# Performance work log

Hardware: AMD Instinct MI355X
Metric: run time of the kernel (lower is better)

Reference implementation:

```python
import jax, jax.numpy as jnp
import numpy as np

EMB = 768
HEADS = 3
HD = EMB // HEADS  # 256
B, S = 4, 2048


def setup_inputs() -> dict:
    key = jax.random.key(0)
    ks = jax.random.split(key, 8)
    inputs_for_keys = jax.random.normal(ks[0], (B, S, EMB), dtype=jnp.float32)
    inputs_for_values = jax.random.normal(ks[1], (B, S, EMB), dtype=jnp.float32)
    inputs_for_queries = jax.random.normal(ks[2], (B, S, EMB), dtype=jnp.float32)
    # stacked per-head projection weights: [heads, emb, head_dim]
    # original uses 'random_uniform' init (small uniform); scale ~0.05
    Wk = jax.random.uniform(ks[3], (HEADS, EMB, HD), jnp.float32, -0.05, 0.05)
    Wv = jax.random.uniform(ks[4], (HEADS, EMB, HD), jnp.float32, -0.05, 0.05)
    Wq = jax.random.uniform(ks[5], (HEADS, EMB, HD), jnp.float32, -0.05, 0.05)
    Wo = jax.random.normal(ks[6], (EMB, EMB), dtype=jnp.float32) * (1.0 / np.sqrt(EMB))
    bo = jnp.zeros((EMB,), dtype=jnp.float32)
    return {
        "inputs_for_keys": inputs_for_keys,
        "inputs_for_values": inputs_for_values,
        "inputs_for_queries": inputs_for_queries,
        "Wk": Wk, "Wv": Wv, "Wq": Wq, "Wo": Wo, "bo": bo,
    }


def reference(inputs_for_keys, inputs_for_values, inputs_for_queries, Wk, Wv, Wq, Wo, bo):
    # per-head projections, batched over heads: [b, h, s, f]
    K = jnp.einsum('bse,hef->bhsf', inputs_for_keys, Wk)
    V = jnp.einsum('bse,hef->bhsf', inputs_for_values, Wv)
    Q = jnp.einsum('bse,hef->bhsf', inputs_for_queries, Wq)

    seq_k = inputs_for_keys.shape[1]
    seq_q = inputs_for_queries.shape[1]
    # NOTE: original scales by sqrt(window_size_keys) (seq len), not sqrt(d_k)
    scale = jnp.sqrt(jnp.float32(seq_k))

    scores = jnp.einsum('bhqf,bhkf->bhqk', Q, K) / scale
    # causal mask: -inf strictly above the diagonal (j > i)
    mask = jnp.triu(jnp.full((seq_q, seq_k), -jnp.inf, dtype=scores.dtype), k=1)
    scores = scores + mask

    attn = jax.nn.softmax(scores, axis=-1)  # [b,h,q,k]
    heads = jnp.einsum('bhqk,bhkf->bhqf', attn, V)

    # concat heads along feature dim: [b, q, heads*hd]
    b, h, q, f = heads.shape
    concat = heads.transpose(0, 2, 1, 3).reshape(b, q, h * f)
    return concat @ Wo + bo
```

## Files before the change

### kernel.cpp

```cpp
#include <hip/hip_runtime.h>

#define BATCH 4
#define NHEADS 3
#define SEQ 2048
#define HDIM 256
#define EMBD 768
#define MTOT (BATCH*SEQ)
#define WSZ (NHEADS*EMBD*HDIM)

typedef unsigned short u16x8 __attribute__((ext_vector_type(8)));
typedef unsigned short u16x4 __attribute__((ext_vector_type(4)));
typedef __bf16 bf16x8 __attribute__((ext_vector_type(8)));
typedef float fx4 __attribute__((ext_vector_type(4)));

__device__ __forceinline__ unsigned short f2bf(float x) {
    union { float f; unsigned int u; } v; v.f = x;
    unsigned int r = v.u + 0x7fffu + ((v.u >> 16) & 1u);
    return (unsigned short)(r >> 16);
}

__device__ __forceinline__ fx4 mfma16(u16x8 a, u16x8 b, fx4 c) {
    return __builtin_amdgcn_mfma_f32_16x16x32_bf16(
        __builtin_bit_cast(bf16x8, a), __builtin_bit_cast(bf16x8, b), c, 0, 0, 0);
}

__device__ __forceinline__ void gl_lds16(const unsigned short* g, unsigned short* l) {
    __builtin_amdgcn_global_load_lds(
        (const __attribute__((address_space(1))) unsigned int*)g,
        (__attribute__((address_space(3))) unsigned int*)l, 16, 0, 0);
}

__device__ const unsigned char attn_sched[48] = {
    124,125, 63, 120,121, 116,117, 59, 112,113, 108,109, 55, 104,105,
    100,101, 51,  96, 97,  92, 93, 47,  88, 89,  84, 85, 43,  80, 81,
     76, 77, 39,  72, 73,  68, 69, 35,  64, 65,  31, 27, 23, 19, 15,
     11,  7,  3
};

__global__ __launch_bounds__(256) void castAw_kernel(
    const float* __restrict__ Ak, const float* __restrict__ Av,
    const float* __restrict__ Aq,
    const float* __restrict__ Wk, const float* __restrict__ Wv,
    const float* __restrict__ Wq, const float* __restrict__ Wo,
    unsigned short* __restrict__ Abf, unsigned short* __restrict__ Wt,
    unsigned short* __restrict__ Wot)
{
    __shared__ float tile[64][65];
    int bx = blockIdx.x;
    if (bx < 9216) {
        int e = (bx * 256 + threadIdx.x) * 8;
        int t = e / (MTOT * EMBD);
        int r = e - t * (MTOT * EMBD);
        const float* A = (t == 0) ? Ak : (t == 1) ? Av : Aq;
        const fx4* s = (const fx4*)(A + r);
        fx4 v0 = s[0], v1 = s[1];
        u16x8 o;
        o[0]=f2bf(v0[0]); o[1]=f2bf(v0[1]); o[2]=f2bf(v0[2]); o[3]=f2bf(v0[3]);
        o[4]=f2bf(v1[0]); o[5]=f2bf(v1[1]); o[6]=f2bf(v1[2]); o[7]=f2bf(v1[3]);
        *(u16x8*)(Abf + e) = o;
        return;
    }
    int z = bx - 9216;
    const float* src; unsigned short* dst;
    int src_ld, dst_ld, e0, f0;
    if (z < 432) {
        int t = z / 144, rem = z - t * 144;
        int h = rem / 48, tl = rem - h * 48;
        e0 = (tl % 12) * 64; f0 = (tl / 12) * 64;
        const float* W = (t == 0) ? Wk : (t == 1) ? Wv : Wq;
        src = W + h * 768 * 256; src_ld = 256;
        dst = Wt + t * WSZ + h * 256 * 768; dst_ld = 768;
    } else {
        int zz = z - 432;
        e0 = (zz % 12) * 64; f0 = (zz / 12) * 64;
        src = Wo; src_ld = 768;
        dst = Wot; dst_ld = 768;
    }
    int tx = threadIdx.x & 63, ty4 = threadIdx.x >> 6;
    #pragma unroll
    for (int i = 0; i < 16; ++i) {
        int r = ty4 + i * 4;
        tile[r][tx] = src[(e0 + r) * src_ld + f0 + tx];
    }
    __syncthreads();
    #pragma unroll
    for (int i = 0; i < 16; ++i) {
        int r = ty4 + i * 4;
        dst[(f0 + r) * dst_ld + e0 + tx] = f2bf(tile[tx][r]);
    }
}

__global__ __launch_bounds__(256) void proj_kernel(
    const unsigned short* __restrict__ Abf, const unsigned short* __restrict__ Wt,
    unsigned short* __restrict__ Kg, unsigned short* __restrict__ Vg,
    unsigned short* __restrict__ Qg)
{
    __shared__ alignas(16) unsigned short S[17408];
    unsigned short* As = S;
    unsigned short* Bs = S + 8192;

    int z = blockIdx.z;
    const unsigned short* A = Abf + z * (MTOT * EMBD);
    int m0 = blockIdx.x * 128;
    int h = blockIdx.y >> 1, fbase = (blockIdx.y & 1) * 128;
    const unsigned short* W = Wt + z * WSZ + (h * 256 + fbase) * EMBD;

    int tid = threadIdx.x;
    int w = tid >> 6, ln = tid & 63;
    int lane16 = ln & 15, quad = ln >> 4;
    int mw = (w & 1) * 64, nw = (w >> 1) * 64;

    fx4 acc[4][4];
    #pragma unroll
    for (int i = 0; i < 4; ++i)
        #pragma unroll
        for (int j = 0; j < 4; ++j) acc[i][j] = (fx4){0.f, 0.f, 0.f, 0.f};

    const unsigned short *Ag[4], *Wg[4];
    #pragma unroll
    for (int i = 0; i < 4; ++i) {
        int c = tid + 256 * i;
        int R = c >> 3;
        int So = (((c & 7) ^ (R & 7)) * 8);
        Ag[i] = A + (m0 + R) * EMBD + So;
        Wg[i] = W + R * EMBD + So;
    }

    int ca0 = ((quad + 0) ^ (lane16 & 7)) * 8;
    int ca1 = ((quad + 4) ^ (lane16 & 7)) * 8;

    for (int kb = 0; kb < EMBD; kb += 64) {
        __syncthreads();
        #pragma unroll
        for (int i = 0; i < 4; ++i) {
            gl_lds16(Ag[i] + kb, &As[(tid + 256 * i) * 8]);
            gl_lds16(Wg[i] + kb, &Bs[(tid + 256 * i) * 8]);
        }
        __syncthreads();

        #pragma unroll
        for (int kh = 0; kh < 2; ++kh) {
            int co = kh ? ca1 : ca0;
            u16x8 af[4], bf[4];
            #pragma unroll
            for (int i = 0; i < 4; ++i) {
                af[i] = *(const u16x8*)&As[(mw + i * 16 + lane16) * 64 + co];
                bf[i] = *(const u16x8*)&Bs[(nw + i * 16 + lane16) * 64 + co];
            }
            #pragma unroll
            for (int i = 0; i < 4; ++i)
                #pragma unroll
                for (int j = 0; j < 4; ++j)
                    acc[i][j] = mfma16(af[i], bf[j], acc[i][j]);
        }
    }

    __syncthreads();
    int b = m0 >> 11, sq0 = m0 & 2047;

    if (z == 1) {
        #pragma unroll
        for (int i = 0; i < 4; ++i)
            #pragma unroll
            for (int j = 0; j < 4; ++j) {
                int fl = nw + j * 16 + lane16;
                int ml = mw + i * 16 + quad * 4;
                u16x4 pk;
                pk[0] = f2bf(acc[i][j][0]); pk[1] = f2bf(acc[i][j][1]);
                pk[2] = f2bf(acc[i][j][2]); pk[3] = f2bf(acc[i][j][3]);
                *(u16x4*)&S[fl * 136 + ml] = pk;
            }
        __syncthreads();
        int fl = tid >> 1, mseg = (tid & 1) * 64;
        const unsigned short* srcp = &S[fl * 136 + mseg];
        unsigned short* dstp = Vg + ((b * NHEADS + h) * HDIM + fbase + fl) * SEQ + sq0 + mseg;
        #pragma unroll
        for (int c = 0; c < 8; ++c)
            *(u16x8*)(dstp + c * 8) = *(const u16x8*)(srcp + c * 8);
    } else {
        #pragma unroll
        for (int i = 0; i < 4; ++i)
            #pragma unroll
            for (int j = 0; j < 4; ++j) {
                int fl = nw + j * 16 + lane16;
                int ml = mw + i * 16 + quad * 4;
                #pragma unroll
                for (int r = 0; r < 4; ++r)
                    S[(ml + r) * 136 + fl] = f2bf(acc[i][j][r]);
            }
        __syncthreads();
        unsigned short* dst0 = (z == 0) ? Kg : Qg;
        int ml = tid >> 1, fseg = (tid & 1) * 64;
        const unsigned short* srcp = &S[ml * 136 + fseg];
        unsigned short* dstp = dst0 + ((b * NHEADS + h) * SEQ + sq0 + ml) * HDIM + fbase + fseg;
        #pragma unroll
        for (int c = 0; c < 8; ++c)
            *(u16x8*)(dstp + c * 8) = *(const u16x8*)(srcp + c * 8);
    }
}

__global__ __launch_bounds__(256) void attn_kernel(
    const unsigned short* __restrict__ Kg, const unsigned short* __restrict__ Vg,
    const unsigned short* __restrict__ Qg, unsigned short* __restrict__ heads,
    float* __restrict__ Opart, float* __restrict__ Lpart)
{
    __shared__ alignas(16) unsigned short Ks[32 * 264];
    __shared__ alignas(16) unsigned short Vs[256 * 40];

    int bx = blockIdx.x;
    int bh = bx % 12;
    int ent = attn_sched[bx / 12];
    int qt = ent >> 2, kc = ent & 3;
    int tid = threadIdx.x;
    int w = tid >> 6, ln = tid & 63;
    int lane16 = ln & 15, quad = ln >> 4;
    int q0w = qt * 64 + w * 16;

    const unsigned short* Kbase = Kg + bh * (SEQ * HDIM);
    const unsigned short* Vbase = Vg + bh * (SEQ * HDIM);
    const unsigned short* Qbase = Qg + bh * (SEQ * HDIM);

    u16x8 qf[8];
    {
        const unsigned short* qrow = Qbase + (q0w + lane16) * HDIM + quad * 8;
        #pragma unroll
        for (int c = 0; c < 8; ++c) qf[c] = *(const u16x8*)(qrow + c * 32);
    }

    fx4 o[16];
    #pragma unroll
    for (int i = 0; i < 16; ++i) o[i] = (fx4){0.f, 0.f, 0.f, 0.f};
    float lsum = 0.f;

    const float Cs2 = 0.03188010519640429f;

    int t0, t1;
    if (kc == 3) { t0 = 0; t1 = 2 * qt + 2; }
    else         { t0 = kc * (qt + 1); t1 = t0 + qt + 1; }

    int ksrow = tid >> 3, kseg = tid & 7;
    const unsigned short* kstage = Kbase + ksrow * HDIM + kseg * 32;
    const unsigned short* vstage = Vbase + tid * SEQ;

    u16x8 kreg[4], vreg[4];
    {
        int k0 = t0 * 32;
        #pragma unroll
        for (int j = 0; j < 4; ++j) {
            kreg[j] = *(const u16x8*)(kstage + k0 * HDIM + j * 8);
            vreg[j] = *(const u16x8*)(vstage + k0 + j * 8);
        }
    }

    for (int kt = t0; kt < t1; ++kt) {
        __syncthreads();
        {
            u16x8* kd = (u16x8*)&Ks[ksrow * 264 + kseg * 32];
            kd[0] = kreg[0]; kd[1] = kreg[1]; kd[2] = kreg[2]; kd[3] = kreg[3];
            u16x8* vd = (u16x8*)&Vs[tid * 40];
            vd[0] = vreg[0]; vd[1] = vreg[1]; vd[2] = vreg[2]; vd[3] = vreg[3];
        }
        if (kt + 1 < t1) {
            int k0n = (kt + 1) * 32;
            #pragma unroll
            for (int j = 0; j < 4; ++j) {
                kreg[j] = *(const u16x8*)(kstage + k0n * HDIM + j * 8);
                vreg[j] = *(const u16x8*)(vstage + k0n + j * 8);
            }
        }
        __syncthreads();

        int k0 = kt * 32;
        fx4 s0 = (fx4){0.f,0.f,0.f,0.f}, s1 = (fx4){0.f,0.f,0.f,0.f};
        #pragma unroll
        for (int c = 0; c < 8; ++c) {
            u16x8 ka = *(const u16x8*)&Ks[lane16 * 264 + c * 32 + quad * 8];
            u16x8 kb = *(const u16x8*)&Ks[(16 + lane16) * 264 + c * 32 + quad * 8];
            s0 = mfma16(ka, qf[c], s0);
            s1 = mfma16(kb, qf[c], s1);
        }

        float p0[4], p1[4];
        int q = q0w + lane16;
        #pragma unroll
        for (int r = 0; r < 4; ++r) {
            int ka_ = k0 + quad * 4 + r;
            float e0 = exp2f(s0[r] * Cs2);
            float e1 = exp2f(s1[r] * Cs2);
            p0[r] = (ka_      <= q) ? e0 : 0.f;
            p1[r] = (ka_ + 16 <= q) ? e1 : 0.f;
            lsum += p0[r] + p1[r];
        }

        u16x8 pf;
        #pragma unroll
        for (int j = 0; j < 8; ++j) {
            int srcLane = ((((quad << 1) + (j >> 2)) & 3) << 4) | lane16;
            float v0 = __shfl(p0[j & 3], srcLane, 64);
            float v1 = __shfl(p1[j & 3], srcLane, 64);
            pf[j] = f2bf(quad >= 2 ? v1 : v0);
        }

        #pragma unroll
        for (int ft = 0; ft < 16; ++ft) {
            u16x8 vf = *(const u16x8*)&Vs[(ft * 16 + lane16) * 40 + quad * 8];
            o[ft] = mfma16(pf, vf, o[ft]);
        }
    }

    lsum += __shfl_xor(lsum, 16, 64);
    lsum += __shfl_xor(lsum, 32, 64);

    if (kc == 3) {
        float linv = 1.f / lsum;
        float inv[4];
        #pragma unroll
        for (int r = 0; r < 4; ++r) inv[r] = __shfl(linv, quad * 4 + r, 64);
        int b = bh / 3, h = bh - (bh / 3) * 3;
        unsigned short* hp = heads + (b * SEQ + q0w + quad * 4) * EMBD + h * HDIM + lane16;
        #pragma unroll
        for (int ft = 0; ft < 16; ++ft)
            #pragma unroll
            for (int r = 0; r < 4; ++r)
                hp[r * EMBD + ft * 16] = f2bf(o[ft][r] * inv[r]);
    } else {
        int slot = (bh * 16 + (qt - 16)) * 2 + kc;
        float* Op = Opart + slot * 16384 + (w * 16 + quad * 4) * 256 + lane16;
        #pragma unroll
        for (int ft = 0; ft < 16; ++ft)
            #pragma unroll
            for (int r = 0; r < 4; ++r)
                Op[r * 256 + ft * 16] = o[ft][r];
        if (quad == 0) Lpart[slot * 64 + w * 16 + lane16] = lsum;
    }
}

__global__ __launch_bounds__(256) void combine_kernel(
    const float* __restrict__ Opart, const float* __restrict__ Lpart,
    unsigned short* __restrict__ heads)
{
    int t = blockIdx.x;
    int bh = t >> 4, qt = (t & 15) + 16;
    int s0 = t * 2, s1 = s0 + 1;
    int tid = threadIdx.x;
    int row = tid >> 2, fseg = (tid & 3) * 64;
    float l = Lpart[s0 * 64 + row] + Lpart[s1 * 64 + row];
    float inv = 1.f / l;
    const fx4* O0 = (const fx4*)(Opart + s0 * 16384 + row * 256 + fseg);
    const fx4* O1 = (const fx4*)(Opart + s1 * 16384 + row * 256 + fseg);
    int b = bh / 3, h = bh - (bh / 3) * 3;
    unsigned short* hp = heads + (b * SEQ + qt * 64 + row) * EMBD + h * HDIM + fseg;
    #pragma unroll
    for (int i = 0; i < 16; ++i) {
        fx4 v = O0[i] + O1[i];
        u16x4 pk;
        pk[0] = f2bf(v[0] * inv); pk[1] = f2bf(v[1] * inv);
        pk[2] = f2bf(v[2] * inv); pk[3] = f2bf(v[3] * inv);
        *(u16x4*)(hp + i * 4) = pk;
    }
}

__global__ __launch_bounds__(256) void outproj_kernel(
    const unsigned short* __restrict__ A, const unsigned short* __restrict__ Wot,
    const float* __restrict__ bo, float* __restrict__ out)
{
    __shared__ alignas(16) unsigned short S[16384];
    unsigned short* As = S;
    unsigned short* Bs = S + 8192;

    int m0 = blockIdx.x * 128, n0 = blockIdx.y * 128;
    int tid = threadIdx.x;
    int w = tid >> 6, ln = tid & 63;
    int lane16 = ln & 15, quad = ln >> 4;
    int mw = (w & 1) * 64, nw = (w >> 1) * 64;

    fx4 acc[4][4];
    #pragma unroll
    for (int i = 0; i < 4; ++i)
        #pragma unroll
        for (int j = 0; j < 4; ++j) acc[i][j] = (fx4){0.f, 0.f, 0.f, 0.f};

    const unsigned short *Ag[4], *Wg[4];
    #pragma unroll
    for (int i = 0; i < 4; ++i) {
        int c = tid + 256 * i;
        int R = c >> 3;
        int So = (((c & 7) ^ (R & 7)) * 8);
        Ag[i] = A + (m0 + R) * EMBD + So;
        Wg[i] = Wot + (n0 + R) * EMBD + So;
    }
    int ca0 = ((quad + 0) ^ (lane16 & 7)) * 8;
    int ca1 = ((quad + 4) ^ (lane16 & 7)) * 8;

    for (int kb = 0; kb < EMBD; kb += 64) {
        __syncthreads();
        #pragma unroll
        for (int i = 0; i < 4; ++i) {
            gl_lds16(Ag[i] + kb, &As[(tid + 256 * i) * 8]);
            gl_lds16(Wg[i] + kb, &Bs[(tid + 256 * i) * 8]);
        }
        __syncthreads();

        #pragma unroll
        for (int kh = 0; kh < 2; ++kh) {
            int co = kh ? ca1 : ca0;
            u16x8 af[4], bf[4];
            #pragma unroll
            for (int i = 0; i < 4; ++i) {
                af[i] = *(const u16x8*)&As[(mw + i * 16 + lane16) * 64 + co];
                bf[i] = *(const u16x8*)&Bs[(nw + i * 16 + lane16) * 64 + co];
            }
            #pragma unroll
            for (int i = 0; i < 4; ++i)
                #pragma unroll
                for (int j = 0; j < 4; ++j)
                    acc[i][j] = mfma16(af[i], bf[j], acc[i][j]);
        }
    }

    #pragma unroll
    for (int i = 0; i < 4; ++i) {
        int mb = m0 + mw + i * 16 + quad * 4;
        #pragma unroll
        for (int j = 0; j < 4; ++j) {
            int n = n0 + nw + j * 16 + lane16;
            float bias = bo[n];
            #pragma unroll
            for (int r = 0; r < 4; ++r)
                out[(mb + r) * EMBD + n] = acc[i][j][r] + bias;
        }
    }
}

extern "C" void kernel_launch(void* const* d_in, const int* in_sizes, int n_in,
                              void* d_out, int out_size, void* d_ws, size_t ws_size,
                              hipStream_t stream) {
    const float* Ak = (const float*)d_in[0];
    const float* Av = (const float*)d_in[1];
    const float* Aq = (const float*)d_in[2];
    const float* Wk = (const float*)d_in[3];
    const float* Wv = (const float*)d_in[4];
    const float* Wq = (const float*)d_in[5];
    const float* Wo = (const float*)d_in[6];
    const float* bo = (const float*)d_in[7];
    float* out = (float*)d_out;

    char* base = (char*)d_ws;
    unsigned short* Wt    = (unsigned short*)(base);
    unsigned short* Wot   = (unsigned short*)(base + 3538944);
    unsigned short* Abf   = (unsigned short*)(base + 4718592);
    unsigned short* Kg    = (unsigned short*)(base + 42467328);
    unsigned short* Vg    = (unsigned short*)(base + 55050240);
    unsigned short* Qg    = (unsigned short*)(base + 67633152);
    unsigned short* heads = (unsigned short*)(base + 80216064);
    float* Opart = (float*)(base + 4718592);
    float* Lpart = (float*)(base + 4718592 + 25165824);

    castAw_kernel<<<dim3(9792), dim3(256), 0, stream>>>(
        Ak, Av, Aq, Wk, Wv, Wq, Wo, Abf, Wt, Wot);
    proj_kernel<<<dim3(64, 6, 3), dim3(256), 0, stream>>>(
        Abf, Wt, Kg, Vg, Qg);
    attn_kernel<<<dim3(576), dim3(256), 0, stream>>>(
        Kg, Vg, Qg, heads, Opart, Lpart);
    combine_kernel<<<dim3(192), dim3(256), 0, stream>>>(Opart, Lpart, heads);
    outproj_kernel<<<dim3(64, 6), dim3(256), 0, stream>>>(heads, Wot, bo, out);
}
```

Measured before the change: 279.4 us.

## Rebalance causal attention split-K: 2-way for mid tiles, 3-way for late tiles

Changes the attention work schedule so query tiles 12-23 are split into two key chunks and tiles 24-31 into three, rather than only splitting the last 16 tiles in two. This gives 720 blocks with more even per-block work, and the combine kernel is extended to reduce 2 or 3 partials. The QK^T loop is also split into two independent accumulator chains, and s_setprio is raised around the MFMA sections. In exchange there are more partial writes and reads. Lpart is moved to the start of the workspace, overlapping the weight buffer Wt, which is presumably dead after projection.

```diff
diff --git a/kernel.cpp b/kernel.cpp
--- a/kernel.cpp
+++ b/kernel.cpp
@@ -30,11 +30,12 @@
         (__attribute__((address_space(3))) unsigned int*)l, 16, 0, 0);
 }
 
-__device__ const unsigned char attn_sched[48] = {
-    124,125, 63, 120,121, 116,117, 59, 112,113, 108,109, 55, 104,105,
-    100,101, 51,  96, 97,  92, 93, 47,  88, 89,  84, 85, 43,  80, 81,
-     76, 77, 39,  72, 73,  68, 69, 35,  64, 65,  31, 27, 23, 19, 15,
-     11,  7,  3
+__device__ const unsigned short attn_sched[60] = {
+    180,376,377, 360,361, 164,344,345,510, 328,329,493,494,508,509,
+    148,312,313,462,476,477,478,492, 296,297,445,446,460,461,
+    132,280,281,414,428,429,430,444, 264,265,397,398,412,413,
+    116,248,249,396, 232,233, 100,216,217, 200,201,
+     84, 68, 52, 36, 20, 4
 };
 
 __global__ __launch_bounds__(256) void castAw_kernel(
@@ -210,7 +211,7 @@
     int bx = blockIdx.x;
     int bh = bx % 12;
     int ent = attn_sched[bx / 12];
-    int qt = ent >> 2, kc = ent & 3;
+    int qt = ent >> 4, nc = (ent >> 2) & 3, ck = ent & 3;
     int tid = threadIdx.x;
     int w = tid >> 6, ln = tid & 63;
     int lane16 = ln & 15, quad = ln >> 4;
@@ -234,9 +235,8 @@
 
     const float Cs2 = 0.03188010519640429f;
 
-    int t0, t1;
-    if (kc == 3) { t0 = 0; t1 = 2 * qt + 2; }
-    else         { t0 = kc * (qt + 1); t1 = t0 + qt + 1; }
+    int n32 = 2 * (qt + 1);
+    int t0 = (ck * n32) / nc, t1 = ((ck + 1) * n32) / nc;
 
     int ksrow = tid >> 3, kseg = tid & 7;
     const unsigned short* kstage = Kbase + ksrow * HDIM + kseg * 32;
@@ -272,13 +272,22 @@
 
         int k0 = kt * 32;
         fx4 s0 = (fx4){0.f,0.f,0.f,0.f}, s1 = (fx4){0.f,0.f,0.f,0.f};
-        #pragma unroll
-        for (int c = 0; c < 8; ++c) {
-            u16x8 ka = *(const u16x8*)&Ks[lane16 * 264 + c * 32 + quad * 8];
-            u16x8 kb = *(const u16x8*)&Ks[(16 + lane16) * 264 + c * 32 + quad * 8];
-            s0 = mfma16(ka, qf[c], s0);
-            s1 = mfma16(kb, qf[c], s1);
-        }
+        fx4 s0b = (fx4){0.f,0.f,0.f,0.f}, s1b = (fx4){0.f,0.f,0.f,0.f};
+        __builtin_amdgcn_s_setprio(1);
+        #pragma unroll
+        for (int c = 0; c < 8; c += 2) {
+            u16x8 ka  = *(const u16x8*)&Ks[lane16 * 264 + c * 32 + quad * 8];
+            u16x8 kb  = *(const u16x8*)&Ks[(16 + lane16) * 264 + c * 32 + quad * 8];
+            u16x8 ka2 = *(const u16x8*)&Ks[lane16 * 264 + (c + 1) * 32 + quad * 8];
+            u16x8 kb2 = *(const u16x8*)&Ks[(16 + lane16) * 264 + (c + 1) * 32 + quad * 8];
+            s0  = mfma16(ka,  qf[c],     s0);
+            s1  = mfma16(kb,  qf[c],     s1);
+            s0b = mfma16(ka2, qf[c + 1], s0b);
+            s1b = mfma16(kb2, qf[c + 1], s1b);
+        }
+        __builtin_amdgcn_s_setprio(0);
+        s0 = s0 + s0b;
+        s1 = s1 + s1b;
 
         float p0[4], p1[4];
         int q = q0w + lane16;
@@ -301,17 +310,19 @@
             pf[j] = f2bf(quad >= 2 ? v1 : v0);
         }
 
+        __builtin_amdgcn_s_setprio(1);
         #pragma unroll
         for (int ft = 0; ft < 16; ++ft) {
             u16x8 vf = *(const u16x8*)&Vs[(ft * 16 + lane16) * 40 + quad * 8];
             o[ft] = mfma16(pf, vf, o[ft]);
         }
+        __builtin_amdgcn_s_setprio(0);
     }
 
     lsum += __shfl_xor(lsum, 16, 64);
     lsum += __shfl_xor(lsum, 32, 64);
 
-    if (kc == 3) {
+    if (nc == 1) {
         float linv = 1.f / lsum;
         float inv[4];
         #pragma unroll
@@ -324,7 +335,8 @@
             for (int r = 0; r < 4; ++r)
                 hp[r * EMBD + ft * 16] = f2bf(o[ft][r] * inv[r]);
     } else {
-        int slot = (bh * 16 + (qt - 16)) * 2 + kc;
+        int local = (qt < 24) ? (qt - 12) * 2 + ck : 24 + (qt - 24) * 3 + ck;
+        int slot = bh * 48 + local;
         float* Op = Opart + slot * 16384 + (w * 16 + quad * 4) * 256 + lane16;
         #pragma unroll
         for (int ft = 0; ft < 16; ++ft)
@@ -340,19 +352,25 @@
     unsigned short* __restrict__ heads)
 {
     int t = blockIdx.x;
-    int bh = t >> 4, qt = (t & 15) + 16;
-    int s0 = t * 2, s1 = s0 + 1;
+    int bh = t / 20, qx = t - bh * 20;
+    int qt = 12 + qx;
+    int nc = (qt < 24) ? 2 : 3;
+    int local = (qt < 24) ? (qt - 12) * 2 : 24 + (qt - 24) * 3;
+    int sbase = bh * 48 + local;
     int tid = threadIdx.x;
     int row = tid >> 2, fseg = (tid & 3) * 64;
-    float l = Lpart[s0 * 64 + row] + Lpart[s1 * 64 + row];
+    float l = Lpart[(sbase + 0) * 64 + row] + Lpart[(sbase + 1) * 64 + row];
+    if (nc == 3) l += Lpart[(sbase + 2) * 64 + row];
     float inv = 1.f / l;
-    const fx4* O0 = (const fx4*)(Opart + s0 * 16384 + row * 256 + fseg);
-    const fx4* O1 = (const fx4*)(Opart + s1 * 16384 + row * 256 + fseg);
+    const fx4* O0 = (const fx4*)(Opart + (sbase + 0) * 16384 + row * 256 + fseg);
+    const fx4* O1 = (const fx4*)(Opart + (sbase + 1) * 16384 + row * 256 + fseg);
+    const fx4* O2 = (const fx4*)(Opart + (sbase + 2) * 16384 + row * 256 + fseg);
     int b = bh / 3, h = bh - (bh / 3) * 3;
     unsigned short* hp = heads + (b * SEQ + qt * 64 + row) * EMBD + h * HDIM + fseg;
     #pragma unroll
     for (int i = 0; i < 16; ++i) {
         fx4 v = O0[i] + O1[i];
+        if (nc == 3) v = v + O2[i];
         u16x4 pk;
         pk[0] = f2bf(v[0] * inv); pk[1] = f2bf(v[1] * inv);
         pk[2] = f2bf(v[2] * inv); pk[3] = f2bf(v[3] * inv);
@@ -454,14 +472,14 @@
     unsigned short* Qg    = (unsigned short*)(base + 67633152);
     unsigned short* heads = (unsigned short*)(base + 80216064);
     float* Opart = (float*)(base + 4718592);
-    float* Lpart = (float*)(base + 4718592 + 25165824);
+    float* Lpart = (float*)(base);
 
     castAw_kernel<<<dim3(9792), dim3(256), 0, stream>>>(
         Ak, Av, Aq, Wk, Wv, Wq, Wo, Abf, Wt, Wot);
     proj_kernel<<<dim3(64, 6, 3), dim3(256), 0, stream>>>(
         Abf, Wt, Kg, Vg, Qg);
-    attn_kernel<<<dim3(576), dim3(256), 0, stream>>>(
+    attn_kernel<<<dim3(720), dim3(256), 0, stream>>>(
         Kg, Vg, Qg, heads, Opart, Lpart);
-    combine_kernel<<<dim3(192), dim3(256), 0, stream>>>(Opart, Lpart, heads);
+    combine_kernel<<<dim3(240), dim3(256), 0, stream>>>(Opart, Lpart, heads);
     outproj_kernel<<<dim3(64, 6), dim3(256), 0, stream>>>(heads, Wot, bo, out);
 }
```

New measurement: 302.1 us. +8.1%, slower.

## Read V fragments directly from global memory and pack P shuffles into bf16 pairs

Applied to the files above, without the earlier changes.

Removes the shared-memory staging buffer for the transposed V tile, so each wave loads its V MFMA operands straight from global memory (L2/L1) inside the PV loop instead of staging through registers and LDS. Separately, the two probability values are converted to bf16 and packed into one 32-bit word before the cross-lane shuffle, halving the shuffle count. This cuts LDS traffic and footprint, which may help occupancy. The cost is that every wave re-reads V from global memory with no prefetch, so the PV MFMAs are exposed to global-load latency and more redundant cache traffic.

```diff
diff --git a/kernel.cpp b/kernel.cpp
--- a/kernel.cpp
+++ b/kernel.cpp
@@ -205,7 +205,6 @@
     float* __restrict__ Opart, float* __restrict__ Lpart)
 {
     __shared__ alignas(16) unsigned short Ks[32 * 264];
-    __shared__ alignas(16) unsigned short Vs[256 * 40];
 
     int bx = blockIdx.x;
     int bh = bx % 12;
@@ -240,16 +239,14 @@
 
     int ksrow = tid >> 3, kseg = tid & 7;
     const unsigned short* kstage = Kbase + ksrow * HDIM + kseg * 32;
-    const unsigned short* vstage = Vbase + tid * SEQ;
-
-    u16x8 kreg[4], vreg[4];
+    const unsigned short* vbaseL = Vbase + lane16 * SEQ + quad * 8;
+
+    u16x8 kreg[4];
     {
         int k0 = t0 * 32;
         #pragma unroll
-        for (int j = 0; j < 4; ++j) {
+        for (int j = 0; j < 4; ++j)
             kreg[j] = *(const u16x8*)(kstage + k0 * HDIM + j * 8);
-            vreg[j] = *(const u16x8*)(vstage + k0 + j * 8);
-        }
     }
 
     for (int kt = t0; kt < t1; ++kt) {
@@ -257,16 +254,12 @@
         {
             u16x8* kd = (u16x8*)&Ks[ksrow * 264 + kseg * 32];
             kd[0] = kreg[0]; kd[1] = kreg[1]; kd[2] = kreg[2]; kd[3] = kreg[3];
-            u16x8* vd = (u16x8*)&Vs[tid * 40];
-            vd[0] = vreg[0]; vd[1] = vreg[1]; vd[2] = vreg[2]; vd[3] = vreg[3];
         }
         if (kt + 1 < t1) {
             int k0n = (kt + 1) * 32;
             #pragma unroll
-            for (int j = 0; j < 4; ++j) {
+            for (int j = 0; j < 4; ++j)
                 kreg[j] = *(const u16x8*)(kstage + k0n * HDIM + j * 8);
-                vreg[j] = *(const u16x8*)(vstage + k0n + j * 8);
-            }
         }
         __syncthreads();
 
@@ -280,30 +273,30 @@
             s1 = mfma16(kb, qf[c], s1);
         }
 
-        float p0[4], p1[4];
+        unsigned int pp[4];
         int q = q0w + lane16;
         #pragma unroll
         for (int r = 0; r < 4; ++r) {
             int ka_ = k0 + quad * 4 + r;
             float e0 = exp2f(s0[r] * Cs2);
             float e1 = exp2f(s1[r] * Cs2);
-            p0[r] = (ka_      <= q) ? e0 : 0.f;
-            p1[r] = (ka_ + 16 <= q) ? e1 : 0.f;
-            lsum += p0[r] + p1[r];
+            float v0 = (ka_      <= q) ? e0 : 0.f;
+            float v1 = (ka_ + 16 <= q) ? e1 : 0.f;
+            lsum += v0 + v1;
+            pp[r] = (unsigned int)f2bf(v0) | ((unsigned int)f2bf(v1) << 16);
         }
 
         u16x8 pf;
         #pragma unroll
         for (int j = 0; j < 8; ++j) {
             int srcLane = ((((quad << 1) + (j >> 2)) & 3) << 4) | lane16;
-            float v0 = __shfl(p0[j & 3], srcLane, 64);
-            float v1 = __shfl(p1[j & 3], srcLane, 64);
-            pf[j] = f2bf(quad >= 2 ? v1 : v0);
+            unsigned int ts = (unsigned int)__shfl((int)pp[j & 3], srcLane, 64);
+            pf[j] = (quad >= 2) ? (unsigned short)(ts >> 16) : (unsigned short)ts;
         }
 
         #pragma unroll
         for (int ft = 0; ft < 16; ++ft) {
-            u16x8 vf = *(const u16x8*)&Vs[(ft * 16 + lane16) * 40 + quad * 8];
+            u16x8 vf = *(const u16x8*)(vbaseL + ft * (16 * SEQ) + k0);
             o[ft] = mfma16(pf, vf, o[ft]);
         }
     }
```

After: 334.8 us. +19.8%, slower.
